# Kernel optimization log

Measured on AMD Instinct MI355X. Metric: run time of the kernel, lower is better.

## Reference

```python
import jax, jax.numpy as jnp
import numpy as np

# Qwen3-Next gated delta-net dims
H_K, H_V, DK, DV = 16, 32, 128, 128
HID, KCONV = 2048, 4
KEY_DIM, VALUE_DIM = H_K * DK, H_V * DV      # 2048, 4096
CONV_DIM = 2 * KEY_DIM + VALUE_DIM           # 8192
GV = H_V // H_K                              # v-heads per k-head = 2
EPS = 1e-6
SEQ = 4096


def setup_inputs() -> dict:
    key = jax.random.key(0)
    ks = jax.random.split(key, 8)
    n = lambda k, sh, s: jax.random.normal(k, sh, jnp.float32) * s
    return {
        "hidden_states": n(ks[0], (SEQ, HID), 1.0),
        "W_qkvz": n(ks[1], (HID, 2 * KEY_DIM + 2 * VALUE_DIM), HID ** -0.5),
        "W_ba": n(ks[2], (HID, 2 * H_V), HID ** -0.5),
        "conv_w": n(ks[3], (CONV_DIM, KCONV), 0.5),
        "A_log": jnp.log(jax.random.uniform(ks[4], (H_V,), jnp.float32, 1.0, 16.0)),
        "dt_bias": jnp.ones((H_V,), jnp.float32),
        "norm_weight": jnp.ones((DV,), jnp.float32),
        "W_out": n(ks[5], (VALUE_DIM, HID), VALUE_DIM ** -0.5),
    }


def _l2norm(x):
    return x * jax.lax.rsqrt(jnp.sum(x * x, -1, keepdims=True) + EPS)


def reference(hidden_states, W_qkvz, W_ba, conv_w, A_log, dt_bias, norm_weight, W_out):
    L = hidden_states.shape[0]
    # 1. input projections
    qkvz = hidden_states @ W_qkvz            # (L, 12288)
    ba = hidden_states @ W_ba                # (L, 64)
    # fix_query_key_value_ordering: view per k-head group then split
    qkvz = qkvz.reshape(L, H_K, 2 * DK + 2 * GV * DV)
    q = qkvz[:, :, :DK]                                         # (L, Hk, dk)
    k = qkvz[:, :, DK:2 * DK]                                   # (L, Hk, dk)
    v = qkvz[:, :, 2 * DK:2 * DK + GV * DV].reshape(L, H_V, DV)  # (L, Hv, dv)
    z = qkvz[:, :, 2 * DK + GV * DV:].reshape(L, H_V, DV)
    ba = ba.reshape(L, H_K, 2 * GV)
    b = ba[:, :, :GV].reshape(L, H_V)
    a = ba[:, :, GV:].reshape(L, H_V)

    # 2. causal depthwise conv1d over [q|k|v] channels + silu
    mixed = jnp.concatenate([q.reshape(L, KEY_DIM), k.reshape(L, KEY_DIM),
                             v.reshape(L, VALUE_DIM)], axis=-1)  # (L, CONV_DIM)
    xp = jnp.pad(mixed, ((KCONV - 1, 0), (0, 0)))
    conv = sum(xp[i:i + L] * conv_w[:, i] for i in range(KCONV))
    mixed = jax.nn.silu(conv)

    q = mixed[:, :KEY_DIM].reshape(L, H_K, DK)
    k = mixed[:, KEY_DIM:2 * KEY_DIM].reshape(L, H_K, DK)
    v = mixed[:, 2 * KEY_DIM:].reshape(L, H_V, DV)

    # 3. fused gating: g = -exp(A_log) * softplus(a + dt_bias); beta = sigmoid(b)
    g = -jnp.exp(A_log) * jax.nn.softplus(a + dt_bias)   # (L, Hv)
    beta = jax.nn.sigmoid(b)                              # (L, Hv)

    # qk l2-norm + scale, expand k-heads to v-heads (GQA repeat)
    q = jnp.repeat(_l2norm(q), GV, axis=1) * (DK ** -0.5)  # (L, Hv, dk)
    k = jnp.repeat(_l2norm(k), GV, axis=1)

    # 4. gated delta-rule recurrence over time (state per head: dk x dv)
    def step(S, inp):
        qt, kt, vt, gt, bt = inp
        S = S * jnp.exp(gt)[:, None, None]
        kv = jnp.einsum('hkv,hk->hv', S, kt)
        delta = (vt - kv) * bt[:, None]
        S = S + kt[:, :, None] * delta[:, None, :]
        return S, jnp.einsum('hkv,hk->hv', S, qt)

    S0 = jnp.zeros((H_V, DK, DV), jnp.float32)
    _, core = jax.lax.scan(step, S0, (q, k, v, g, beta))   # (L, Hv, dv)

    # 5. gated RMSNorm (norm before gate): rmsnorm(x)*w * silu(z)
    var = jnp.mean(core * core, -1, keepdims=True)
    core = core * jax.lax.rsqrt(var + EPS) * norm_weight
    core = core * jax.nn.silu(z)

    # 6. output projection
    return core.reshape(L, VALUE_DIM) @ W_out
```

## Files before the change

kernel.cpp:

```cpp
#include <hip/hip_runtime.h>
#include <hip/hip_bf16.h>

#define SEQ 4096
#define HID 2048
#define HK_ 16
#define HV_ 32
#define KEY_DIM 2048
#define VALUE_DIM 4096
#define CONV_DIM 8192
#define NQKVZ 12288

typedef unsigned short ushort_t;
typedef short bf16x8 __attribute__((ext_vector_type(8)));
typedef float f32x4 __attribute__((ext_vector_type(4)));
typedef float f32x2 __attribute__((ext_vector_type(2)));

__device__ __forceinline__ float bf2f(ushort_t h) {
    union { unsigned int u; float f; } x; x.u = ((unsigned int)h) << 16; return x.f;
}
__device__ __forceinline__ void cvt8(uint4 v, float* f) {
    unsigned int w[4] = {v.x, v.y, v.z, v.w};
#pragma unroll
    for (int i = 0; i < 4; i++) {
        union { unsigned int u; float f; } lo, hi;
        lo.u = w[i] << 16; hi.u = w[i] & 0xffff0000u;
        f[2 * i] = lo.f; f[2 * i + 1] = hi.f;
    }
}
__device__ __forceinline__ void cvt8v(uint4 v, f32x2* f) {
    unsigned int w[4] = {v.x, v.y, v.z, v.w};
#pragma unroll
    for (int i = 0; i < 4; i++) {
        union { unsigned int u; float f; } lo, hi;
        lo.u = w[i] << 16; hi.u = w[i] & 0xffff0000u;
        f[i] = (f32x2){lo.f, hi.f};
    }
}
__device__ __forceinline__ ushort_t f2bf(float f) {
    union { float f; unsigned int u; } x; x.f = f;
    unsigned int u = x.u;
    u += 0x7fffu + ((u >> 16) & 1u);
    return (ushort_t)(u >> 16);
}

__device__ __forceinline__ void gload_lds16(const void* g, void* l) {
    __builtin_amdgcn_global_load_lds(
        (const __attribute__((address_space(1))) void*)g,
        (__attribute__((address_space(3))) void*)l, 16, 0, 0);
}

template <int CTRL>
__device__ __forceinline__ float dpp_add(float x) {
    union { float f; int i; } a, b;
    a.f = x;
    b.i = __builtin_amdgcn_update_dpp(0, a.i, CTRL, 0xF, 0xF, true);
    return a.f + b.f;
}
__device__ __forceinline__ float red16(float x) {
    x = dpp_add<0xB1>(x);
    x = dpp_add<0x4E>(x);
    x = dpp_add<0x141>(x);
    x = dpp_add<0x140>(x);
    return x;
}

__global__ void k_cvt(const float* __restrict__ src, ushort_t* __restrict__ dst)
{
    size_t i = ((size_t)blockIdx.x * 256 + threadIdx.x) * 8;
    float4 a = *(const float4*)&src[i];
    float4 b = *(const float4*)&src[i + 4];
    ushort_t u[8];
    u[0]=f2bf(a.x); u[1]=f2bf(a.y); u[2]=f2bf(a.z); u[3]=f2bf(a.w);
    u[4]=f2bf(b.x); u[5]=f2bf(b.y); u[6]=f2bf(b.z); u[7]=f2bf(b.w);
    *(uint4*)&dst[i] = *(uint4*)u;
}

__global__ __launch_bounds__(256) void k_transpose(const float* __restrict__ src,
                                                   ushort_t* __restrict__ dst,
                                                   int R, int C)
{
    __shared__ float tile[64][65];
    int c0 = blockIdx.x * 64, r0 = blockIdx.y * 64;
    int t = threadIdx.x;
    int tr = t >> 4, tc = (t & 15) * 4;
#pragma unroll
    for (int r = 0; r < 4; r++) {
        float4 v = *(const float4*)&src[(size_t)(r0 + tr + r * 16) * C + c0 + tc];
        tile[tr + r * 16][tc + 0] = v.x;
        tile[tr + r * 16][tc + 1] = v.y;
        tile[tr + r * 16][tc + 2] = v.z;
        tile[tr + r * 16][tc + 3] = v.w;
    }
    __syncthreads();
#pragma unroll
    for (int r = 0; r < 4; r++) {
        int n = c0 + tr + r * 16;
        ushort_t u[4];
#pragma unroll
        for (int i = 0; i < 4; i++) u[i] = f2bf(tile[tc + i][tr + r * 16]);
        *(uint2*)&dst[(size_t)n * R + r0 + tc] = *(uint2*)u;
    }
}

__global__ void k_ba(const float* __restrict__ A, const float* __restrict__ B,
                     const float* __restrict__ A_log, const float* __restrict__ dt_bias,
                     float* __restrict__ gbf)
{
    __shared__ float As[16][132];
    __shared__ float Bs[16][68];
    int tid = threadIdx.x;
    int m0 = blockIdx.x * 128;
    int tx = tid & 15, ty = tid >> 4;
    int arow = tid >> 2, akq = tid & 3;
    int brow = tid >> 4, bc4 = tid & 15;
    float acc[8][4];
#pragma unroll
    for (int i = 0; i < 8; i++)
#pragma unroll
        for (int j = 0; j < 4; j++) acc[i][j] = 0.f;

    for (int k0 = 0; k0 < HID; k0 += 16) {
        float4 a0 = *(const float4*)&A[(size_t)(m0 + arow) * HID + k0 + akq * 4];
        float4 a1 = *(const float4*)&A[(size_t)(m0 + arow + 64) * HID + k0 + akq * 4];
        float4 b0 = *(const float4*)&B[(size_t)(k0 + brow) * 64 + bc4 * 4];
        __syncthreads();
        As[akq * 4 + 0][arow] = a0.x; As[akq * 4 + 1][arow] = a0.y;
        As[akq * 4 + 2][arow] = a0.z; As[akq * 4 + 3][arow] = a0.w;
        As[akq * 4 + 0][arow + 64] = a1.x; As[akq * 4 + 1][arow + 64] = a1.y;
        As[akq * 4 + 2][arow + 64] = a1.z; As[akq * 4 + 3][arow + 64] = a1.w;
        *(float4*)&Bs[brow][bc4 * 4] = b0;
        __syncthreads();
#pragma unroll
        for (int kk = 0; kk < 16; kk++) {
            float xa[8], yb[4];
            *(float4*)&xa[0] = *(const float4*)&As[kk][ty * 8];
            *(float4*)&xa[4] = *(const float4*)&As[kk][ty * 8 + 4];
            *(float4*)&yb[0] = *(const float4*)&Bs[kk][tx * 4];
#pragma unroll
            for (int i = 0; i < 8; i++)
#pragma unroll
                for (int j = 0; j < 4; j++) acc[i][j] += xa[i] * yb[j];
        }
    }
#pragma unroll
    for (int i = 0; i < 8; i++) {
        int t = m0 + ty * 8 + i;
#pragma unroll
        for (int j = 0; j < 4; j++) {
            int c = tx * 4 + j;
            int hk = c >> 2, rr = c & 3;
            float val = acc[i][j];
            if (rr < 2) {
                int hv = hk * 2 + rr;
                gbf[(t * HV_ + hv) * 2 + 1] = 1.f / (1.f + expf(-val));
            } else {
                int hv = hk * 2 + (rr - 2);
                float v2 = val + dt_bias[hv];
                float sp = (v2 > 20.f) ? v2 : log1pf(expf(v2));
                float g = -expf(A_log[hv]) * sp;
                gbf[(t * HV_ + hv) * 2 + 0] = expf(g);
            }
        }
    }
}

__global__ __launch_bounds__(256) void k_gemm_qkvz(const ushort_t* __restrict__ Ab,
                                                   const ushort_t* __restrict__ Bt,
                                                   ushort_t* __restrict__ preact,
                                                   ushort_t* __restrict__ zb)
{
    __shared__ ushort_t As[128][32];
    __shared__ ushort_t Bs[128][32];
    int tid = threadIdx.x;
    int m0 = blockIdx.y * 128, n0 = blockIdx.x * 128;
    int lane = tid & 63, wave = tid >> 6;
    int wm = (wave >> 1) * 64, wn = (wave & 1) * 64;
    int quad = lane >> 4, l16 = lane & 15;

    int srow = ((wave & 1) << 6) + (lane >> 2);
    int scol = (lane & 3) << 3;
    const ushort_t* gsrc = (wave < 2)
        ? &Ab[(size_t)(m0 + srow) * HID + scol]
        : &Bt[(size_t)(n0 + srow) * HID + scol];
    ushort_t* lbase = ((wave < 2) ? &As[0][0] : &Bs[0][0]) + ((wave & 1) << 11);

    f32x4 acc[4][4];
#pragma unroll
    for (int i = 0; i < 4; i++)
#pragma unroll
        for (int j = 0; j < 4; j++) acc[i][j] = (f32x4){0.f, 0.f, 0.f, 0.f};

    for (int k0 = 0; k0 < HID; k0 += 32) {
#pragma unroll
        for (int i = 0; i < 4; i++)
            gload_lds16(gsrc + k0 + (size_t)i * 16 * HID, lbase + i * 512);
        __syncthreads();
        bf16x8 af[4], bfr[4];
#pragma unroll
        for (int i = 0; i < 4; i++) af[i]  = *(bf16x8*)&As[wm + i * 16 + l16][quad * 8];
#pragma unroll
        for (int j = 0; j < 4; j++) bfr[j] = *(bf16x8*)&Bs[wn + j * 16 + l16][quad * 8];
#pragma unroll
        for (int i = 0; i < 4; i++)
#pragma unroll
            for (int j = 0; j < 4; j++)
                acc[i][j] = __builtin_amdgcn_mfma_f32_16x16x32_bf16(af[i], bfr[j], acc[i][j], 0, 0, 0);
        __syncthreads();
    }
    int hk = n0 / 768, r = n0 % 768;
    ushort_t* dst; int ldd;
    if (r < 128)      { dst = preact + hk * 128;                    ldd = CONV_DIM; }
    else if (r < 256) { dst = preact + 2048 + hk * 128;             ldd = CONV_DIM; }
    else if (r < 512) { dst = preact + 4096 + hk * 256 + (r - 256); ldd = CONV_DIM; }
    else              { dst = zb + hk * 256 + (r - 512);            ldd = VALUE_DIM; }
#pragma unroll
    for (int i = 0; i < 4; i++)
#pragma unroll
        for (int j = 0; j < 4; j++)
#pragma unroll
            for (int rg = 0; rg < 4; rg++) {
                int m = m0 + wm + i * 16 + quad * 4 + rg;
                int n = wn + j * 16 + l16;
                dst[(size_t)m * ldd + n] = f2bf(acc[i][j][rg]);
            }
}

__global__ __launch_bounds__(256) void k_gemm_out(const ushort_t* __restrict__ Ab,
                                                  const ushort_t* __restrict__ Bt,
                                                  float* __restrict__ C)
{
    __shared__ ushort_t As[128][32];
    __shared__ ushort_t Bs[128][32];
    int tid = threadIdx.x;
    int m0 = blockIdx.y * 128, n0 = blockIdx.x * 128;
    int lane = tid & 63, wave = tid >> 6;
    int wm = (wave >> 1) * 64, wn = (wave & 1) * 64;
    int quad = lane >> 4, l16 = lane & 15;

    int srow = ((wave & 1) << 6) + (lane >> 2);
    int scol = (lane & 3) << 3;
    const ushort_t* gsrc = (wave < 2)
        ? &Ab[(size_t)(m0 + srow) * VALUE_DIM + scol]
        : &Bt[(size_t)(n0 + srow) * VALUE_DIM + scol];
    ushort_t* lbase = ((wave < 2) ? &As[0][0] : &Bs[0][0]) + ((wave & 1) << 11);

    f32x4 acc[4][4];
#pragma unroll
    for (int i = 0; i < 4; i++)
#pragma unroll
        for (int j = 0; j < 4; j++) acc[i][j] = (f32x4){0.f, 0.f, 0.f, 0.f};

    for (int k0 = 0; k0 < VALUE_DIM; k0 += 32) {
#pragma unroll
        for (int i = 0; i < 4; i++)
            gload_lds16(gsrc + k0 + (size_t)i * 16 * VALUE_DIM, lbase + i * 512);
        __syncthreads();
        bf16x8 af[4], bfr[4];
#pragma unroll
        for (int i = 0; i < 4; i++) af[i]  = *(bf16x8*)&As[wm + i * 16 + l16][quad * 8];
#pragma unroll
        for (int j = 0; j < 4; j++) bfr[j] = *(bf16x8*)&Bs[wn + j * 16 + l16][quad * 8];
#pragma unroll
        for (int i = 0; i < 4; i++)
#pragma unroll
            for (int j = 0; j < 4; j++)
                acc[i][j] = __builtin_amdgcn_mfma_f32_16x16x32_bf16(af[i], bfr[j], acc[i][j], 0, 0, 0);
        __syncthreads();
    }
#pragma unroll
    for (int i = 0; i < 4; i++)
#pragma unroll
        for (int j = 0; j < 4; j++)
#pragma unroll
            for (int rg = 0; rg < 4; rg++) {
                int m = m0 + wm + i * 16 + quad * 4 + rg;
                int n = n0 + wn + j * 16 + l16;
                C[(size_t)m * HID + n] = acc[i][j][rg];
            }
}

__global__ __launch_bounds__(256) void k_conv(const ushort_t* __restrict__ pre,
                                              const float* __restrict__ cw,
                                              ushort_t* __restrict__ qn,
                                              ushort_t* __restrict__ kn,
                                              ushort_t* __restrict__ vv)
{
    int tid = threadIdx.x;
    int c = blockIdx.x * 2048 + tid * 8;
    int t0 = blockIdx.y * 4;
    float w[8][4];
#pragma unroll
    for (int j = 0; j < 8; j++)
        *(float4*)w[j] = *(const float4*)&cw[(size_t)(c + j) * 4];
    float p[7][8];
#pragma unroll
    for (int i = 0; i < 7; i++) {
        int tt = t0 + i - 3;
        if (tt >= 0) {
            uint4 v = *(const uint4*)&pre[(size_t)tt * CONV_DIM + c];
            cvt8(v, p[i]);
        } else {
#pragma unroll
            for (int j = 0; j < 8; j++) p[i][j] = 0.f;
        }
    }
    float x[4][8];
#pragma unroll
    for (int u = 0; u < 4; u++)
#pragma unroll
        for (int j = 0; j < 8; j++) {
            float a = p[u][j] * w[j][0] + p[u + 1][j] * w[j][1]
                    + p[u + 2][j] * w[j][2] + p[u + 3][j] * w[j][3];
            x[u][j] = a / (1.f + expf(-a));
        }
    if (blockIdx.x < 2) {
        bool isq = (blockIdx.x == 0);
        float headscale = isq ? 0.08838834764831845f : 1.f;
        ushort_t* dst = isq ? qn : kn;
        int cc = isq ? c : (c - KEY_DIM);
#pragma unroll
        for (int u = 0; u < 4; u++) {
            float ss = 0.f;
#pragma unroll
            for (int j = 0; j < 8; j++) ss += x[u][j] * x[u][j];
            ss = red16(ss);
            float mul = headscale / sqrtf(ss + 1e-6f);
            ushort_t o[8];
#pragma unroll
            for (int j = 0; j < 8; j++) o[j] = f2bf(x[u][j] * mul);
            *(uint4*)&dst[(size_t)(t0 + u) * KEY_DIM + cc] = *(uint4*)o;
        }
    } else {
        int cc = c - 2 * KEY_DIM;
#pragma unroll
        for (int u = 0; u < 4; u++) {
            ushort_t o[8];
#pragma unroll
            for (int j = 0; j < 8; j++) o[j] = f2bf(x[u][j]);
            *(uint4*)&vv[(size_t)(t0 + u) * VALUE_DIM + cc] = *(uint4*)o;
        }
    }
}

__device__ __forceinline__ void recur_step(f32x2 S[4],
    uint4& rk, uint4& rq, ushort_t& rv, float2& rgb,
    const ushort_t* kp, const ushort_t* qp, const ushort_t* vp,
    const float2* gb, int h, int tpre, float* outp, bool lead)
{
    f32x2 k2[4], q2[4];
    cvt8v(rk, k2);
    cvt8v(rq, q2);
    float v_ = bf2f(rv);
    float e = rgb.x, b = rgb.y;
    rk = *(const uint4*)(kp + (size_t)tpre * KEY_DIM);
    rq = *(const uint4*)(qp + (size_t)tpre * KEY_DIM);
    rv = vp[(size_t)tpre * VALUE_DIM];
    rgb = gb[tpre * HV_ + h];

    f32x2 acc = S[0] * k2[0];
    acc += S[1] * k2[1];
    acc += S[2] * k2[2];
    acc += S[3] * k2[3];
    float d1 = red16(acc.x + acc.y);
    float dl = (v_ - e * d1) * b;
    f32x2 e2  = (f32x2){e, e};
    f32x2 dl2 = (f32x2){dl, dl};
    f32x2 oacc = (f32x2){0.f, 0.f};
#pragma unroll
    for (int j = 0; j < 4; j++) {
        S[j] = S[j] * e2 + k2[j] * dl2;
        oacc += S[j] * q2[j];
    }
    float o = red16(oacc.x + oacc.y);
    if (lead) *outp = o;
}

__global__ __launch_bounds__(256) void k_recur(const ushort_t* __restrict__ qn,
                                               const ushort_t* __restrict__ kn,
                                               const ushort_t* __restrict__ vv,
                                               const float2* __restrict__ gb,
                                               float* __restrict__ core)
{
    int h = blockIdx.y;
    int hk = h >> 1;
    int kc = threadIdx.x & 15;
    int cl = threadIdx.x >> 4;
    int col = blockIdx.x * 16 + cl;
    int kqoff = hk * 128 + kc * 8;
    bool lead = (kc == 0);

    const ushort_t* kp = kn + kqoff;
    const ushort_t* qp = qn + kqoff;
    const ushort_t* vp = vv + h * 128 + col;
    float* outp = core + h * 128 + col;

    f32x2 S[4];
#pragma unroll
    for (int j = 0; j < 4; j++) S[j] = (f32x2){0.f, 0.f};

    uint4 rka = *(const uint4*)kp;
    uint4 rqa = *(const uint4*)qp;
    ushort_t rva = vp[0];
    float2 gba = gb[h];
    uint4 rkb = *(const uint4*)(kp + KEY_DIM);
    uint4 rqb = *(const uint4*)(qp + KEY_DIM);
    ushort_t rvb = vp[VALUE_DIM];
    float2 gbb = gb[HV_ + h];
    uint4 rkc = *(const uint4*)(kp + 2 * KEY_DIM);
    uint4 rqc = *(const uint4*)(qp + 2 * KEY_DIM);
    ushort_t rvc = vp[2 * VALUE_DIM];
    float2 gbc = gb[2 * HV_ + h];
    uint4 rkd = *(const uint4*)(kp + 3 * KEY_DIM);
    uint4 rqd = *(const uint4*)(qp + 3 * KEY_DIM);
    ushort_t rvd = vp[3 * VALUE_DIM];
    float2 gbd = gb[3 * HV_ + h];

    for (int t = 0; t < SEQ; t += 4) {
        int tp = (t <= SEQ - 8) ? (t + 4) : t;
        recur_step(S, rka, rqa, rva, gba, kp, qp, vp, gb, h, tp,
                   outp + (size_t)t * VALUE_DIM, lead);
        recur_step(S, rkb, rqb, rvb, gbb, kp, qp, vp, gb, h, tp + 1,
                   outp + (size_t)(t + 1) * VALUE_DIM, lead);
        recur_step(S, rkc, rqc, rvc, gbc, kp, qp, vp, gb, h, tp + 2,
                   outp + (size_t)(t + 2) * VALUE_DIM, lead);
        recur_step(S, rkd, rqd, rvd, gbd, kp, qp, vp, gb, h, tp + 3,
                   outp + (size_t)(t + 3) * VALUE_DIM, lead);
    }
}

__global__ void k_gate(const float* __restrict__ core, const ushort_t* __restrict__ z,
                       const float* __restrict__ nw, ushort_t* __restrict__ corebf)
{
    __shared__ float red[2];
    int hv = blockIdx.x, t = blockIdx.y, d = threadIdx.x;
    size_t idx = (size_t)t * VALUE_DIM + hv * 128 + d;
    float cval = core[idx];
    float ss = cval * cval;
    for (int m = 32; m >= 1; m >>= 1) ss += __shfl_xor(ss, m, 64);
    int wv = d >> 6, ln = d & 63;
    if (ln == 0) red[wv] = ss;
    __syncthreads();
    float var = (red[0] + red[1]) * (1.f / 128.f);
    float zv = bf2f(z[idx]);
    float out = cval * (1.f / sqrtf(var + 1e-6f)) * nw[d] * (zv / (1.f + expf(-zv)));
    corebf[idx] = f2bf(out);
}

extern "C" void kernel_launch(void* const* d_in, const int* in_sizes, int n_in,
                              void* d_out, int out_size, void* d_ws, size_t ws_size,
                              hipStream_t stream)
{
    const float* hs    = (const float*)d_in[0];
    const float* Wqkvz = (const float*)d_in[1];
    const float* Wba   = (const float*)d_in[2];
    const float* convw = (const float*)d_in[3];
    const float* Alog  = (const float*)d_in[4];
    const float* dtb   = (const float*)d_in[5];
    const float* nw    = (const float*)d_in[6];
    const float* Wout  = (const float*)d_in[7];
    float* out = (float*)d_out;

    char* w = (char*)d_ws;
    ushort_t* preact = (ushort_t*)w;
    float*    coreb  = (float*)w;
    w += (size_t)SEQ * CONV_DIM * 2;
    ushort_t* zb = (ushort_t*)w;  w += (size_t)SEQ * VALUE_DIM * 2;
    float* gbf   = (float*)w;     w += (size_t)SEQ * HV_ * 8;
    ushort_t* qnb = (ushort_t*)w; w += (size_t)SEQ * KEY_DIM * 2;
    ushort_t* knb = (ushort_t*)w; w += (size_t)SEQ * KEY_DIM * 2;
    ushort_t* vvb = (ushort_t*)w; w += (size_t)SEQ * VALUE_DIM * 2;
    size_t needed = (size_t)(w - (char*)d_ws);
    if (ws_size < needed) return;

    ushort_t* wqT    = qnb;
    ushort_t* hsb    = qnb + (size_t)24 * 1024 * 1024;
    ushort_t* woutT  = vvb;
    ushort_t* corebf = qnb;

    hipLaunchKernelGGL(k_ba, dim3(32), dim3(256), 0, stream, hs, Wba, Alog, dtb, gbf);
    hipLaunchKernelGGL(k_cvt, dim3(4096), dim3(256), 0, stream, hs, hsb);
    hipLaunchKernelGGL(k_transpose, dim3(192, 32), dim3(256), 0, stream, Wqkvz, wqT, HID, NQKVZ);
    hipLaunchKernelGGL(k_gemm_qkvz, dim3(96, 32), dim3(256), 0, stream, hsb, wqT, preact, zb);
    hipLaunchKernelGGL(k_conv, dim3(4, 1024), dim3(256), 0, stream, preact, convw, qnb, knb, vvb);
    hipLaunchKernelGGL(k_recur, dim3(8, 32), dim3(256), 0, stream, qnb, knb, vvb,
                       (const float2*)gbf, coreb);
    hipLaunchKernelGGL(k_transpose, dim3(32, 64), dim3(256), 0, stream, Wout, woutT, VALUE_DIM, HID);
    hipLaunchKernelGGL(k_gate, dim3(32, 4096), dim3(128), 0, stream, coreb, zb, nw, corebf);
    hipLaunchKernelGGL(k_gemm_out, dim3(16, 32), dim3(256), 0, stream, corebf, woutT, out);
}
```

Baseline: 1.764 ms.

## Stage recurrence inputs through double-buffered LDS chunks via async global-to-LDS loads

The recurrence kernel previously prefetched per-timestep k/q/v/gate values into registers four steps ahead straight from global memory. It now copies 32-timestep chunks of K, Q, V and gate/beta into double-buffered shared memory using global_load_lds, so the next chunk loads while the current one is computed. This aims to hide global-memory latency on the serial critical path, at the cost of LDS reads every step and a block-wide barrier per chunk. Correctness depends on the async LDS writes being complete before the barrier, and the code adds no explicit wait for them.

```diff
diff --git a/kernel.cpp b/kernel.cpp
--- a/kernel.cpp
+++ b/kernel.cpp
@@ -47,6 +47,11 @@
     __builtin_amdgcn_global_load_lds(
         (const __attribute__((address_space(1))) void*)g,
         (__attribute__((address_space(3))) void*)l, 16, 0, 0);
+}
+__device__ __forceinline__ void gload_lds4(const void* g, void* l) {
+    __builtin_amdgcn_global_load_lds(
+        (const __attribute__((address_space(1))) void*)g,
+        (__attribute__((address_space(3))) void*)l, 4, 0, 0);
 }
 
 template <int CTRL>
@@ -342,89 +347,98 @@
     }
 }
 
-__device__ __forceinline__ void recur_step(f32x2 S[4],
-    uint4& rk, uint4& rq, ushort_t& rv, float2& rgb,
-    const ushort_t* kp, const ushort_t* qp, const ushort_t* vp,
-    const float2* gb, int h, int tpre, float* outp, bool lead)
-{
-    f32x2 k2[4], q2[4];
-    cvt8v(rk, k2);
-    cvt8v(rq, q2);
-    float v_ = bf2f(rv);
-    float e = rgb.x, b = rgb.y;
-    rk = *(const uint4*)(kp + (size_t)tpre * KEY_DIM);
-    rq = *(const uint4*)(qp + (size_t)tpre * KEY_DIM);
-    rv = vp[(size_t)tpre * VALUE_DIM];
-    rgb = gb[tpre * HV_ + h];
-
-    f32x2 acc = S[0] * k2[0];
-    acc += S[1] * k2[1];
-    acc += S[2] * k2[2];
-    acc += S[3] * k2[3];
-    float d1 = red16(acc.x + acc.y);
-    float dl = (v_ - e * d1) * b;
-    f32x2 e2  = (f32x2){e, e};
-    f32x2 dl2 = (f32x2){dl, dl};
-    f32x2 oacc = (f32x2){0.f, 0.f};
-#pragma unroll
-    for (int j = 0; j < 4; j++) {
-        S[j] = S[j] * e2 + k2[j] * dl2;
-        oacc += S[j] * q2[j];
-    }
-    float o = red16(oacc.x + oacc.y);
-    if (lead) *outp = o;
-}
-
 __global__ __launch_bounds__(256) void k_recur(const ushort_t* __restrict__ qn,
                                                const ushort_t* __restrict__ kn,
                                                const ushort_t* __restrict__ vv,
                                                const float2* __restrict__ gb,
                                                float* __restrict__ core)
 {
+    __shared__ ushort_t Ks[2][32][128];
+    __shared__ ushort_t Qs[2][32][128];
+    __shared__ ushort_t Vs[2][32][16];
+    __shared__ float    Gs[2][32][2];
+    int tid = threadIdx.x;
     int h = blockIdx.y;
     int hk = h >> 1;
-    int kc = threadIdx.x & 15;
-    int cl = threadIdx.x >> 4;
-    int col = blockIdx.x * 16 + cl;
-    int kqoff = hk * 128 + kc * 8;
+    int kc = tid & 15;
+    int cl = tid >> 4;
     bool lead = (kc == 0);
-
-    const ushort_t* kp = kn + kqoff;
-    const ushort_t* qp = qn + kqoff;
-    const ushort_t* vp = vv + h * 128 + col;
-    float* outp = core + h * 128 + col;
-
-    f32x2 S[4];
-#pragma unroll
-    for (int j = 0; j < 4; j++) S[j] = (f32x2){0.f, 0.f};
-
-    uint4 rka = *(const uint4*)kp;
-    uint4 rqa = *(const uint4*)qp;
-    ushort_t rva = vp[0];
-    float2 gba = gb[h];
-    uint4 rkb = *(const uint4*)(kp + KEY_DIM);
-    uint4 rqb = *(const uint4*)(qp + KEY_DIM);
-    ushort_t rvb = vp[VALUE_DIM];
-    float2 gbb = gb[HV_ + h];
-    uint4 rkc = *(const uint4*)(kp + 2 * KEY_DIM);
-    uint4 rqc = *(const uint4*)(qp + 2 * KEY_DIM);
-    ushort_t rvc = vp[2 * VALUE_DIM];
-    float2 gbc = gb[2 * HV_ + h];
-    uint4 rkd = *(const uint4*)(kp + 3 * KEY_DIM);
-    uint4 rqd = *(const uint4*)(qp + 3 * KEY_DIM);
-    ushort_t rvd = vp[3 * VALUE_DIM];
-    float2 gbd = gb[3 * HV_ + h];
-
-    for (int t = 0; t < SEQ; t += 4) {
-        int tp = (t <= SEQ - 8) ? (t + 4) : t;
-        recur_step(S, rka, rqa, rva, gba, kp, qp, vp, gb, h, tp,
-                   outp + (size_t)t * VALUE_DIM, lead);
-        recur_step(S, rkb, rqb, rvb, gbb, kp, qp, vp, gb, h, tp + 1,
-                   outp + (size_t)(t + 1) * VALUE_DIM, lead);
-        recur_step(S, rkc, rqc, rvc, gbc, kp, qp, vp, gb, h, tp + 2,
-                   outp + (size_t)(t + 2) * VALUE_DIM, lead);
-        recur_step(S, rkd, rqd, rvd, gbd, kp, qp, vp, gb, h, tp + 3,
-                   outp + (size_t)(t + 3) * VALUE_DIM, lead);
+    int lane = tid & 63, wave = tid >> 6;
+
+    const ushort_t* kh = kn + hk * 128;
+    const ushort_t* qh = qn + hk * 128;
+    const ushort_t* vh = vv + h * 128 + blockIdx.x * 16;
+    const float*    gh = (const float*)(gb + h);
+    float* outp = core + h * 128 + blockIdx.x * 16 + cl;
+
+    auto stage = [&](int bi, int t0) {
+        if (wave < 2) {
+            int rb = wave * 16;
+#pragma unroll
+            for (int c = 0; c < 4; c++) {
+                int r = rb + c * 4 + (lane >> 4);
+                gload_lds16(kh + (size_t)(t0 + r) * KEY_DIM + (lane & 15) * 8,
+                            &Ks[bi][rb + c * 4][0]);
+            }
+#pragma unroll
+            for (int c = 0; c < 2; c++) {
+                int r = rb + c * 8 + (lane >> 3);
+                gload_lds4(vh + (size_t)(t0 + r) * VALUE_DIM + (lane & 7) * 2,
+                           &Vs[bi][rb + c * 8][0]);
+            }
+        } else {
+            int rb = (wave - 2) * 16;
+#pragma unroll
+            for (int c = 0; c < 4; c++) {
+                int r = rb + c * 4 + (lane >> 4);
+                gload_lds16(qh + (size_t)(t0 + r) * KEY_DIM + (lane & 15) * 8,
+                            &Qs[bi][rb + c * 4][0]);
+            }
+            if (wave == 2) {
+                int r = lane >> 1;
+                gload_lds4(gh + (size_t)(t0 + r) * (HV_ * 2) + (lane & 1),
+                           &Gs[bi][0][0]);
+            }
+        }
+    };
+
+    f32x2 S_[4];
+#pragma unroll
+    for (int j = 0; j < 4; j++) S_[j] = (f32x2){0.f, 0.f};
+
+    stage(0, 0);
+    __syncthreads();
+
+    for (int tc = 0; tc < SEQ / 32; tc++) {
+        int bi = tc & 1;
+        if (tc + 1 < SEQ / 32) stage(bi ^ 1, (tc + 1) * 32);
+        int t0 = tc * 32;
+#pragma unroll 8
+        for (int s = 0; s < 32; s++) {
+            uint4 kvr = *(const uint4*)&Ks[bi][s][kc * 8];
+            uint4 qvr = *(const uint4*)&Qs[bi][s][kc * 8];
+            f32x2 k2[4], q2[4];
+            cvt8v(kvr, k2);
+            cvt8v(qvr, q2);
+            float v_ = bf2f(Vs[bi][s][cl]);
+            float e = Gs[bi][s][0], b = Gs[bi][s][1];
+            f32x2 acc = S_[0] * k2[0];
+            acc += S_[1] * k2[1];
+            acc += S_[2] * k2[2];
+            acc += S_[3] * k2[3];
+            float d1 = red16(acc.x + acc.y);
+            float dl = (v_ - e * d1) * b;
+            f32x2 e2 = (f32x2){e, e}, dl2 = (f32x2){dl, dl};
+            f32x2 oacc = (f32x2){0.f, 0.f};
+#pragma unroll
+            for (int j = 0; j < 4; j++) {
+                S_[j] = S_[j] * e2 + k2[j] * dl2;
+                oacc += S_[j] * q2[j];
+            }
+            float o = red16(oacc.x + oacc.y);
+            if (lead) outp[(size_t)(t0 + s) * VALUE_DIM] = o;
+        }
+        __syncthreads();
     }
 }
 
```

Result: faster. 1.561 ms, median of 2 (-11.5%).
